# Kernel optimization log

Measured on AMD Instinct MI355X. Metric: run time of the kernel, lower is better.

## Reference

```python
import jax, jax.numpy as jnp
import numpy as np

H = 128  # hidden_size == input_size

def setup_inputs() -> dict:
    key = jax.random.key(0)
    ks = jax.random.split(key, 8)
    T, B = 512, 1024
    s = 1.0 / np.sqrt(H)
    return {
        "input": jax.random.normal(ks[0], (T, B, H), dtype=jnp.float32),
        "initial_h": jax.random.normal(ks[1], (B, H), dtype=jnp.float32),
        "w_ih": jax.random.uniform(ks[2], (3 * H, H), jnp.float32, -s, s),
        "w_hh": jax.random.uniform(ks[3], (3 * H, H), jnp.float32, -s, s),
        "b_ih": jax.random.uniform(ks[4], (3 * H,), jnp.float32, -s, s),
        "b_hh": jax.random.uniform(ks[5], (3 * H,), jnp.float32, -s, s),
        "w_out": jax.random.uniform(ks[6], (1, H), jnp.float32, -s, s),
        "b_out": jax.random.uniform(ks[7], (1,), jnp.float32, -s, s),
    }

def reference(input, initial_h, w_ih, w_hh, b_ih, b_hh, w_out, b_out):
    # Pre-batch all input-to-hidden GEMMs: [T, B, 3H]
    xg = jnp.einsum("tbi,gi->tbg", input, w_ih) + b_ih

    def step(h, xg_t):
        hg = h @ w_hh.T + b_hh                       # [B, 3H]
        xr, xz, xn = jnp.split(xg_t, 3, axis=-1)
        hr, hz, hn = jnp.split(hg, 3, axis=-1)
        r = jax.nn.sigmoid(xr + hr)
        z = jax.nn.sigmoid(xz + hz)
        n = jnp.tanh(xn + r * hn)
        h_new = (1.0 - z) * n + z * h
        return h_new, None

    h, _ = jax.lax.scan(step, initial_h, xg)
    return h @ w_out.T + b_out                        # [B, 1]
```

## Files before the change

kernel.cpp:

```cpp
#include <hip/hip_runtime.h>

#define T_STEPS 512
#define BATCH   1024
#define HID     128
#define BHID    (BATCH * HID)

typedef __attribute__((ext_vector_type(8))) short short8;
typedef __attribute__((ext_vector_type(4))) float f32x4;

__device__ __forceinline__ unsigned cvtpk_bf16(float lo, float hi) {
    unsigned r;
    asm("v_cvt_pk_bf16_f32 %0, %1, %2" : "=v"(r) : "v"(lo), "v"(hi));
    return r;
}
__device__ __forceinline__ float fast_sigmoid(float x) {
    return __builtin_amdgcn_rcpf(1.0f + __builtin_amdgcn_exp2f(-1.442695041f * x));
}
__device__ __forceinline__ float fast_tanh(float x) {
    return 1.0f - 2.0f * __builtin_amdgcn_rcpf(1.0f + __builtin_amdgcn_exp2f(2.885390082f * x));
}
__device__ __forceinline__ void barrier_lgkm() {
    __builtin_amdgcn_sched_barrier(0);
    asm volatile("s_waitcnt lgkmcnt(0)" ::: "memory");
    __builtin_amdgcn_sched_barrier(0);
    __builtin_amdgcn_s_barrier();
    __builtin_amdgcn_sched_barrier(0);
}

__global__ __launch_bounds__(512, 2) void gru_scan(
    const float* __restrict__ x, const float* __restrict__ h0,
    const float* __restrict__ w_ih, const float* __restrict__ w_hh,
    const float* __restrict__ b_ih, const float* __restrict__ b_hh,
    const float* __restrict__ w_out, const float* __restrict__ b_out,
    float* __restrict__ out)
{
    __shared__ unsigned hbf[2 * 1024];
    __shared__ float red[16][8];

    const int tid = threadIdx.x;
    const int w   = tid >> 6;
    const int l   = tid & 63;
    const int lm  = l & 15;
    const int lg  = l >> 4;
    const int b0  = blockIdx.x << 4;
    const int col = w * 16 + lm;

    short8 wih[3][4], whh[3][4];
    float biasX[3], biasH[3];
    #pragma unroll
    for (int f = 0; f < 3; ++f) {
        const int n = f * 128 + col;
        biasX[f] = b_ih[n];
        biasH[f] = b_hh[n];
        #pragma unroll
        for (int kf = 0; kf < 4; ++kf) {
            const int koff = kf * 32 + lg * 8;
            union { short8 s; unsigned u[4]; } p;
            {
                const float4 a = *(const float4*)(w_ih + n * HID + koff);
                const float4 b = *(const float4*)(w_ih + n * HID + koff + 4);
                p.u[0] = cvtpk_bf16(a.x, a.y); p.u[1] = cvtpk_bf16(a.z, a.w);
                p.u[2] = cvtpk_bf16(b.x, b.y); p.u[3] = cvtpk_bf16(b.z, b.w);
                wih[f][kf] = p.s;
            }
            {
                const float4 a = *(const float4*)(w_hh + n * HID + koff);
                const float4 b = *(const float4*)(w_hh + n * HID + koff + 4);
                p.u[0] = cvtpk_bf16(a.x, a.y); p.u[1] = cvtpk_bf16(a.z, a.w);
                p.u[2] = cvtpk_bf16(b.x, b.y); p.u[3] = cvtpk_bf16(b.z, b.w);
                whh[f][kf] = p.s;
            }
        }
    }

    const unsigned* ha_rd[4];
    #pragma unroll
    for (int kf = 0; kf < 4; ++kf) {
        const int bo = (kf * 64 + lg * 16) ^ ((lm & 7) << 4);
        ha_rd[kf] = &hbf[lm * 64 + (bo >> 2)];
    }
    short* h_wr[4];
    #pragma unroll
    for (int r = 0; r < 4; ++r) {
        const int row = lg * 4 + r;
        const int byte = (col * 2) ^ ((row & 7) << 4);
        h_wr[r] = (short*)hbf + row * 128 + (byte >> 1);
    }

    int loA[4], loB[4];
    #pragma unroll
    for (int kf = 0; kf < 4; ++kf) {
        loA[kf] = lm * HID + kf * 32 + lg * 8;
        loB[kf] = loA[kf] + 4;
    }
    const float* xrow = x + (size_t)b0 * HID;

    float hreg[4];
    #pragma unroll
    for (int r = 0; r < 4; ++r) {
        const int row = lg * 4 + r;
        hreg[r] = h0[(size_t)(b0 + row) * HID + col];
        *(short*)((char*)h_wr[r] + 0) = (short)cvtpk_bf16(hreg[r], hreg[r]);
    }

    float4 xnA[4], xnB[4];
    #pragma unroll
    for (int kf = 0; kf < 4; ++kf) {
        xnA[kf] = *(const float4*)(xrow + loA[kf]);
        xnB[kf] = *(const float4*)(xrow + loB[kf]);
    }

    __syncthreads();

#define GRU_STEP(P, TCUR) do {                                                  \
                                              \
    short8 ha[4];                                                               \
    _Pragma("unroll")                                                           \
    for (int kf = 0; kf < 4; ++kf)                                              \
        ha[kf] = *(const short8*)((const char*)ha_rd[kf] + (P) * 4096);         \
            \
    short8 xa[4];                                                               \
    _Pragma("unroll")                                                           \
    for (int kf = 0; kf < 4; ++kf) {                                            \
        union { short8 s; unsigned u[4]; } p;                                   \
        p.u[0] = cvtpk_bf16(xnA[kf].x, xnA[kf].y);                              \
        p.u[1] = cvtpk_bf16(xnA[kf].z, xnA[kf].w);                              \
        p.u[2] = cvtpk_bf16(xnB[kf].x, xnB[kf].y);                              \
        p.u[3] = cvtpk_bf16(xnB[kf].z, xnB[kf].w);                              \
        xa[kf] = p.s;                                                           \
    }                                                                           \
                 \
    {                                                                           \
        const int tn = ((TCUR) + 1 < T_STEPS) ? (TCUR) + 1 : (TCUR);            \
        const float* xt = xrow + (size_t)tn * BHID;                             \
        _Pragma("unroll")                                                       \
        for (int kf = 0; kf < 4; ++kf) {                                        \
            xnA[kf] = *(const float4*)(xt + loA[kf]);                           \
            xnB[kf] = *(const float4*)(xt + loB[kf]);                           \
        }                                                                       \
    }                                                                           \
                                          \
    f32x4 accX[3], accH[3];                                                     \
    _Pragma("unroll")                                                           \
    for (int f = 0; f < 3; ++f) {                                               \
        accX[f] = (f32x4){biasX[f], biasX[f], biasX[f], biasX[f]};              \
        accH[f] = (f32x4){biasH[f], biasH[f], biasH[f], biasH[f]};              \
        _Pragma("unroll")                                                       \
        for (int kf = 0; kf < 4; ++kf) {                                        \
            accX[f] = __builtin_amdgcn_mfma_f32_16x16x32_bf16(xa[kf], wih[f][kf], accX[f], 0, 0, 0); \
            accH[f] = __builtin_amdgcn_mfma_f32_16x16x32_bf16(ha[kf], whh[f][kf], accH[f], 0, 0, 0); \
        }                                                                       \
    }                                                                           \
                     \
    _Pragma("unroll")                                                           \
    for (int r = 0; r < 4; ++r) {                                               \
        const float pr = accX[0][r] + accH[0][r];                               \
        const float pz = accX[1][r] + accH[1][r];                               \
        const float rr = fast_sigmoid(pr);                                      \
        const float zz = fast_sigmoid(pz);                                      \
        const float nn = fast_tanh(accX[2][r] + rr * accH[2][r]);               \
        const float hn = nn + zz * (hreg[r] - nn);                              \
        hreg[r] = hn;                                                           \
        *(short*)((char*)h_wr[r] + ((P) ^ 1) * 4096) = (short)cvtpk_bf16(hn, hn); \
    }                                                                           \
    barrier_lgkm();                                                             \
} while (0)

    #pragma unroll 1
    for (int t = 0; t < T_STEPS; t += 2) {
        GRU_STEP(0, t);
        GRU_STEP(1, t + 1);
    }
#undef GRU_STEP

    {
        const float wv = w_out[col];
        float s0 = hreg[0] * wv, s1 = hreg[1] * wv, s2 = hreg[2] * wv, s3 = hreg[3] * wv;
        #pragma unroll
        for (int mask = 8; mask >= 1; mask >>= 1) {
            s0 += __shfl_xor(s0, mask);
            s1 += __shfl_xor(s1, mask);
            s2 += __shfl_xor(s2, mask);
            s3 += __shfl_xor(s3, mask);
        }
        if (lm == 0) {
            red[lg * 4 + 0][w] = s0;
            red[lg * 4 + 1][w] = s1;
            red[lg * 4 + 2][w] = s2;
            red[lg * 4 + 3][w] = s3;
        }
    }
    __syncthreads();
    if (tid < 16) {
        float acc = b_out[0];
        #pragma unroll
        for (int j = 0; j < 8; ++j) acc += red[tid][j];
        out[b0 + tid] = acc;
    }
}

extern "C" void kernel_launch(void* const* d_in, const int* in_sizes, int n_in,
                              void* d_out, int out_size, void* d_ws, size_t ws_size,
                              hipStream_t stream) {
    const float* x     = (const float*)d_in[0];
    const float* h0    = (const float*)d_in[1];
    const float* w_ih  = (const float*)d_in[2];
    const float* w_hh  = (const float*)d_in[3];
    const float* b_ih  = (const float*)d_in[4];
    const float* b_hh  = (const float*)d_in[5];
    const float* w_out = (const float*)d_in[6];
    const float* b_out = (const float*)d_in[7];
    gru_scan<<<64, 512, 0, stream>>>(x, h0, w_ih, w_hh, b_ih, b_hh, w_out, b_out, (float*)d_out);
}
```

Measured before the change: 1.170 ms.

## Software-pipeline input GEMM one step ahead of recurrent gate math

Each step now computes the input-projection MFMAs for the next timestep after the recurrent MFMAs, and prefetches x two steps ahead into double-buffered registers. The x-projection for step t is ready before the step starts, so the gate math depends only on the hidden-state MFMAs on the critical path. The input-side MFMAs can then fill gaps while the recurrent MFMA chain drains. The cost is more live registers (two accumulator sets and two x buffers), which risks occupancy loss or spills.

```diff
diff --git a/kernel.cpp b/kernel.cpp
--- a/kernel.cpp
+++ b/kernel.cpp
@@ -103,62 +103,95 @@
         *(short*)((char*)h_wr[r] + 0) = (short)cvtpk_bf16(hreg[r], hreg[r]);
     }
 
-    float4 xnA[4], xnB[4];
+    float4 xb0A[4], xb0B[4], xb1A[4], xb1B[4];
     #pragma unroll
     for (int kf = 0; kf < 4; ++kf) {
-        xnA[kf] = *(const float4*)(xrow + loA[kf]);
-        xnB[kf] = *(const float4*)(xrow + loB[kf]);
+        xb0A[kf] = *(const float4*)(xrow + loA[kf]);
+        xb0B[kf] = *(const float4*)(xrow + loB[kf]);
+    }
+    f32x4 accXa[3], accXb[3];
+    {
+        short8 xa[4];
+        #pragma unroll
+        for (int kf = 0; kf < 4; ++kf) {
+            union { short8 s; unsigned u[4]; } p;
+            p.u[0] = cvtpk_bf16(xb0A[kf].x, xb0A[kf].y);
+            p.u[1] = cvtpk_bf16(xb0A[kf].z, xb0A[kf].w);
+            p.u[2] = cvtpk_bf16(xb0B[kf].x, xb0B[kf].y);
+            p.u[3] = cvtpk_bf16(xb0B[kf].z, xb0B[kf].w);
+            xa[kf] = p.s;
+        }
+        #pragma unroll
+        for (int f = 0; f < 3; ++f) {
+            accXa[f] = (f32x4){biasX[f], biasX[f], biasX[f], biasX[f]};
+            #pragma unroll
+            for (int kf = 0; kf < 4; ++kf)
+                accXa[f] = __builtin_amdgcn_mfma_f32_16x16x32_bf16(xa[kf], wih[f][kf], accXa[f], 0, 0, 0);
+        }
+    }
+    {
+        const float* xt = xrow + (size_t)1 * BHID;
+        #pragma unroll
+        for (int kf = 0; kf < 4; ++kf) {
+            xb1A[kf] = *(const float4*)(xt + loA[kf]);
+            xb1B[kf] = *(const float4*)(xt + loB[kf]);
+        }
     }
 
     __syncthreads();
 
-#define GRU_STEP(P, TCUR) do {                                                  \
-                                              \
+#define GRU_STEP(P, TCUR, XC, XN, XCA, XCB, XLA, XLB) do {                      \
     short8 ha[4];                                                               \
     _Pragma("unroll")                                                           \
     for (int kf = 0; kf < 4; ++kf)                                              \
         ha[kf] = *(const short8*)((const char*)ha_rd[kf] + (P) * 4096);         \
-            \
-    short8 xa[4];                                                               \
-    _Pragma("unroll")                                                           \
-    for (int kf = 0; kf < 4; ++kf) {                                            \
-        union { short8 s; unsigned u[4]; } p;                                   \
-        p.u[0] = cvtpk_bf16(xnA[kf].x, xnA[kf].y);                              \
-        p.u[1] = cvtpk_bf16(xnA[kf].z, xnA[kf].w);                              \
-        p.u[2] = cvtpk_bf16(xnB[kf].x, xnB[kf].y);                              \
-        p.u[3] = cvtpk_bf16(xnB[kf].z, xnB[kf].w);                              \
-        xa[kf] = p.s;                                                           \
-    }                                                                           \
-                 \
+                \
     {                                                                           \
-        const int tn = ((TCUR) + 1 < T_STEPS) ? (TCUR) + 1 : (TCUR);            \
+        const int tn = ((TCUR) + 2 < T_STEPS) ? (TCUR) + 2 : T_STEPS - 1;       \
         const float* xt = xrow + (size_t)tn * BHID;                             \
         _Pragma("unroll")                                                       \
         for (int kf = 0; kf < 4; ++kf) {                                        \
-            xnA[kf] = *(const float4*)(xt + loA[kf]);                           \
-            xnB[kf] = *(const float4*)(xt + loB[kf]);                           \
+            XLA[kf] = *(const float4*)(xt + loA[kf]);                           \
+            XLB[kf] = *(const float4*)(xt + loB[kf]);                           \
         }                                                                       \
     }                                                                           \
-                                          \
-    f32x4 accX[3], accH[3];                                                     \
+                                         \
+    f32x4 accH[3];                                                              \
     _Pragma("unroll")                                                           \
     for (int f = 0; f < 3; ++f) {                                               \
-        accX[f] = (f32x4){biasX[f], biasX[f], biasX[f], biasX[f]};              \
         accH[f] = (f32x4){biasH[f], biasH[f], biasH[f], biasH[f]};              \
         _Pragma("unroll")                                                       \
+        for (int kf = 0; kf < 4; ++kf)                                          \
+            accH[f] = __builtin_amdgcn_mfma_f32_16x16x32_bf16(ha[kf], whh[f][kf], accH[f], 0, 0, 0); \
+    }                                                                           \
+            \
+    {                                                                           \
+        short8 xa[4];                                                           \
+        _Pragma("unroll")                                                       \
         for (int kf = 0; kf < 4; ++kf) {                                        \
-            accX[f] = __builtin_amdgcn_mfma_f32_16x16x32_bf16(xa[kf], wih[f][kf], accX[f], 0, 0, 0); \
-            accH[f] = __builtin_amdgcn_mfma_f32_16x16x32_bf16(ha[kf], whh[f][kf], accH[f], 0, 0, 0); \
+            union { short8 s; unsigned u[4]; } p;                               \
+            p.u[0] = cvtpk_bf16(XCA[kf].x, XCA[kf].y);                          \
+            p.u[1] = cvtpk_bf16(XCA[kf].z, XCA[kf].w);                          \
+            p.u[2] = cvtpk_bf16(XCB[kf].x, XCB[kf].y);                          \
+            p.u[3] = cvtpk_bf16(XCB[kf].z, XCB[kf].w);                          \
+            xa[kf] = p.s;                                                       \
         }                                                                       \
-    }                                                                           \
-                     \
+        _Pragma("unroll")                                                       \
+        for (int f = 0; f < 3; ++f) {                                           \
+            XN[f] = (f32x4){biasX[f], biasX[f], biasX[f], biasX[f]};            \
+            _Pragma("unroll")                                                   \
+            for (int kf = 0; kf < 4; ++kf)                                      \
+                XN[f] = __builtin_amdgcn_mfma_f32_16x16x32_bf16(xa[kf], wih[f][kf], XN[f], 0, 0, 0); \
+        }                                                                       \
+    }                                                                           \
+                                    \
     _Pragma("unroll")                                                           \
     for (int r = 0; r < 4; ++r) {                                               \
-        const float pr = accX[0][r] + accH[0][r];                               \
-        const float pz = accX[1][r] + accH[1][r];                               \
+        const float pr = XC[0][r] + accH[0][r];                                 \
+        const float pz = XC[1][r] + accH[1][r];                                 \
         const float rr = fast_sigmoid(pr);                                      \
         const float zz = fast_sigmoid(pz);                                      \
-        const float nn = fast_tanh(accX[2][r] + rr * accH[2][r]);               \
+        const float nn = fast_tanh(XC[2][r] + rr * accH[2][r]);                 \
         const float hn = nn + zz * (hreg[r] - nn);                              \
         hreg[r] = hn;                                                           \
         *(short*)((char*)h_wr[r] + ((P) ^ 1) * 4096) = (short)cvtpk_bf16(hn, hn); \
@@ -168,8 +201,8 @@
 
     #pragma unroll 1
     for (int t = 0; t < T_STEPS; t += 2) {
-        GRU_STEP(0, t);
-        GRU_STEP(1, t + 1);
+        GRU_STEP(0, t,     accXa, accXb, xb1A, xb1B, xb0A, xb0B);
+        GRU_STEP(1, t + 1, accXb, accXa, xb0A, xb0B, xb1A, xb1B);
     }
 #undef GRU_STEP
 
```

Result: no change. 1.173 ms (+0.2%).
